# Kernel tuning notes

Measured on AMD Instinct MI355X. Metric: run time of the kernel, lower is better.

Reference implementation:

```python
import jax, jax.numpy as jnp
import numpy as np

N = 50000   # nodes
E = 800000  # edges (before self-loops)
IN = 128    # input feature dim
H = 4       # attention heads


def setup_inputs() -> dict:
    key = jax.random.key(0)
    ks = jax.random.split(key, 32)
    f = lambda k, s: (jax.random.normal(k, s, dtype=jnp.float32) * 0.1)
    inp = {
        "x": jax.random.normal(ks[0], (N, IN), dtype=jnp.float32),
        "edge_index": jax.random.randint(ks[1], (2, E), 0, N, dtype=jnp.int32),
        "edge_attr": jax.random.normal(ks[2], (E, 1), dtype=jnp.float32),
        # GATConv 1: 128 -> 8 per head, 4 heads (concat -> 32)
        "W1": f(ks[3], (IN, 32)), "as1": f(ks[4], (H, 8)), "ad1": f(ks[5], (H, 8)), "b1": jnp.zeros((32,), jnp.float32),
        # GATConv 2: 32 -> 16 per head (concat -> 64)
        "W2": f(ks[6], (32, 64)), "as2": f(ks[7], (H, 16)), "ad2": f(ks[8], (H, 16)), "b2": jnp.zeros((64,), jnp.float32),
        # GATConv 3: 64 -> 32 per head (concat -> 128)
        "W3": f(ks[9], (64, 128)), "as3": f(ks[10], (H, 32)), "ad3": f(ks[11], (H, 32)), "b3": jnp.zeros((128,), jnp.float32),
        # GATConv 4: 128 -> 64 per head (concat -> 256)
        "W4": f(ks[12], (128, 256)), "as4": f(ks[13], (H, 64)), "ad4": f(ks[14], (H, 64)), "b4": jnp.zeros((256,), jnp.float32),
        # MLP head
        "Wr": f(ks[15], (256, 32)), "br": jnp.zeros((32,), jnp.float32),
        "Wf1": f(ks[16], (32, 64)), "bf1": jnp.zeros((64,), jnp.float32),
        "Wf2": f(ks[17], (64, 1)), "bf2": jnp.zeros((1,), jnp.float32),
    }
    return inp


def _gat_layer(x, W, a_src, a_dst, bias, src, dst):
    """PyG GATConv (concat=True, negative_slope=0.2, self-loops appended upstream)."""
    heads, C = a_src.shape
    h = (x @ W).reshape(-1, heads, C)              # [N, H, C]
    alpha_s = jnp.sum(h * a_src[None], axis=-1)    # [N, H]
    alpha_d = jnp.sum(h * a_dst[None], axis=-1)    # [N, H]
    e = jax.nn.leaky_relu(alpha_s[src] + alpha_d[dst], 0.2)  # [E', H]
    # segment softmax over incoming edges of each destination node
    emax = jax.ops.segment_max(e, dst, num_segments=N)
    ee = jnp.exp(e - emax[dst])
    denom = jax.ops.segment_sum(ee, dst, num_segments=N)
    alpha = ee / denom[dst]                        # [E', H]
    msg = h[src] * alpha[:, :, None]               # [E', H, C]
    out = jax.ops.segment_sum(msg, dst, num_segments=N)  # [N, H, C]
    return out.reshape(-1, heads * C) + bias


def reference(x, edge_index, edge_attr,
              W1, as1, ad1, b1, W2, as2, ad2, b2,
              W3, as3, ad3, b3, W4, as4, ad4, b4,
              Wr, br, Wf1, bf1, Wf2, bf2):
    # edge_attr is accepted but unused, matching the original forward.
    loop = jnp.arange(N, dtype=edge_index.dtype)
    src = jnp.concatenate([edge_index[0], loop])   # add self-loops (PyG default)
    dst = jnp.concatenate([edge_index[1], loop])
    h = jax.nn.elu(_gat_layer(x, W1, as1, ad1, b1, src, dst))
    h = jax.nn.elu(_gat_layer(h, W2, as2, ad2, b2, src, dst))
    h = jax.nn.elu(_gat_layer(h, W3, as3, ad3, b3, src, dst))
    h = jax.nn.elu(_gat_layer(h, W4, as4, ad4, b4, src, dst))
    h = jax.nn.elu(h @ Wr + br)
    h = jax.nn.elu(h @ Wf1 + bf1)
    return h @ Wf2 + bf2                           # [N, 1]
```

## Files before the change

### kernel.cpp

```cpp
#include <hip/hip_runtime.h>
#include <hip/hip_fp16.h>
#include <math.h>

constexpr int NN = 50000;
constexpr int NE = 800000;
constexpr int NEP = NE + NN;
constexpr int CAP = 96;
constexpr int SCAT_B = (NEP + 255) / 256;
constexpr int PACK_B = 26;
constexpr int NT = (NN + 63) / 64;

typedef _Float16 half8_t __attribute__((ext_vector_type(8)));
typedef float    f32x4_t __attribute__((ext_vector_type(4)));

__device__ __forceinline__ float lrelu02(float x) { return x > 0.f ? x : 0.2f * x; }
__device__ __forceinline__ float eluf(float x)    { return x > 0.f ? x : (__expf(x) - 1.f); }
__device__ __forceinline__ float pick4(float4 q, int hd) {
  return (hd == 0) ? q.x : (hd == 1) ? q.y : (hd == 2) ? q.z : q.w;
}


__device__ __forceinline__ void pack_w_one(const float* __restrict__ W,
                                           __half* __restrict__ Wp,
                                           int M, int tid, int total) {
  if (tid >= total) return;
  int CT = M >> 4;
  int l = tid & 63;
  int c = (tid >> 6) % CT;
  int kc = (tid >> 6) / CT;
  int n = l & 15, q = l >> 4;
  __half* dst = Wp + (size_t)tid * 8;
  const float* src = W + (size_t)(kc * 32 + q * 8) * M + c * 16 + n;
  #pragma unroll
  for (int j = 0; j < 8; j++) dst[j] = __float2half_rn(src[j * M]);
}


template<int M, int C, int CT>
__device__ __forceinline__ void alpha_epilogue(const f32x4_t* acc,
    const float* __restrict__ a_src, const float* __restrict__ a_dst,
    int row_base, int m, float* __restrict__ as_out, float* __restrict__ ad_out) {
  float aS[CT], aD[CT];
  #pragma unroll
  for (int c = 0; c < CT; c++) { aS[c] = a_src[c * 16 + m]; aD[c] = a_dst[c * 16 + m]; }

  if constexpr (C == 8) {
    #pragma unroll
    for (int r = 0; r < 4; r++) {
      float p0 = acc[0][r] * aS[0], p1 = acc[1][r] * aS[1];
      float q0 = acc[0][r] * aD[0], q1 = acc[1][r] * aD[1];
      #pragma unroll
      for (int off = 1; off < 8; off <<= 1) {
        p0 += __shfl_xor(p0, off); p1 += __shfl_xor(p1, off);
        q0 += __shfl_xor(q0, off); q1 += __shfl_xor(q1, off);
      }
      int row = row_base + r;
      if ((m & 7) == 0 && row < NN) {
        int hb = m >> 3;
        as_out[row * 4 + hb]     = p0;
        as_out[row * 4 + 2 + hb] = p1;
        ad_out[row * 4 + hb]     = q0;
        ad_out[row * 4 + 2 + hb] = q1;
      }
    }
  } else {
    constexpr int FPH = C / 16;
    #pragma unroll
    for (int r = 0; r < 4; r++) {
      float bs[4] = {0.f, 0.f, 0.f, 0.f}, bd[4] = {0.f, 0.f, 0.f, 0.f};
      #pragma unroll
      for (int c = 0; c < CT; c++) {
        int hd = c / FPH;
        bs[hd] += acc[c][r] * aS[c];
        bd[hd] += acc[c][r] * aD[c];
      }
      #pragma unroll
      for (int off = 1; off < 16; off <<= 1)
        #pragma unroll
        for (int h = 0; h < 4; h++) {
          bs[h] += __shfl_xor(bs[h], off);
          bd[h] += __shfl_xor(bd[h], off);
        }
      int row = row_base + r;
      if (m < 4 && row < NN) {
        float vs = (m == 0) ? bs[0] : (m == 1) ? bs[1] : (m == 2) ? bs[2] : bs[3];
        float vd = (m == 0) ? bd[0] : (m == 1) ? bd[1] : (m == 2) ? bd[2] : bd[3];
        as_out[row * 4 + m] = vs;
        ad_out[row * 4 + m] = vd;
      }
    }
  }
}


__global__ __launch_bounds__(256) void front_kernel(
    const int* __restrict__ edge_src, const int* __restrict__ edge_dst,
    int* __restrict__ count, int* __restrict__ csr_src,
    const float* __restrict__ W1,
    const float* __restrict__ W2, __half* __restrict__ Wp2,
    const float* __restrict__ W3, __half* __restrict__ Wp3,
    const float* __restrict__ W4, __half* __restrict__ Wp4,
    const float* __restrict__ Wr, __half* __restrict__ Wrp,
    const float* __restrict__ Wf1, __half* __restrict__ Wf1p,
    const float* __restrict__ x, __half* __restrict__ Ch,
    const float* __restrict__ a_src, const float* __restrict__ a_dst,
    float* __restrict__ as_out, float* __restrict__ ad_out) {
  int b = blockIdx.x;
  if (b < SCAT_B) {
    int i = b * 256 + threadIdx.x;
    if (i < NEP) {
      int s, d;
      if (i < NE) { s = edge_src[i]; d = edge_dst[i]; } else { s = i - NE; d = s; }
      int pos = atomicAdd(&count[d], 1);
      if (pos < CAP) csr_src[d * CAP + pos] = s;
    }
    return;
  }
  if (b < SCAT_B + PACK_B) {
    int tid = (b - SCAT_B) * 256 + threadIdx.x;
    if (tid < 256)            pack_w_one(W2, Wp2, 64,  tid,        256);
    else if (tid < 1280)      pack_w_one(W3, Wp3, 128, tid - 256,  1024);
    else if (tid < 5376)      pack_w_one(W4, Wp4, 256, tid - 1280, 4096);
    else if (tid < 6400)      pack_w_one(Wr, Wrp, 32,  tid - 5376, 1024);
    else if (tid < 6656)      pack_w_one(Wf1, Wf1p, 64, tid - 6400, 256);
    return;
  }

  constexpr int M = 32, K = 128, CT = 2, KC = 4;
  __shared__ _Float16 Ah[64 * 40];
  __shared__ _Float16 Bs[KC * CT * 64 * 8];
  int t = threadIdx.x;
  int w = t >> 6, l = t & 63;
  int m = l & 15, q = l >> 4;
  int row0 = (b - SCAT_B - PACK_B) * 64;

  #pragma unroll
  for (int u0 = 0; u0 < 2; u0++) {
    int u = t + u0 * 256;
    int ul = u & 63;
    int uc = (u >> 6) & 1;
    int ukc = u >> 7;
    int un = ul & 15, uq = ul >> 4;
    const float* src = W1 + (size_t)(ukc * 32 + uq * 8) * M + uc * 16 + un;
    _Float16* dst = &Bs[u * 8];
    #pragma unroll
    for (int j = 0; j < 8; j++) dst[j] = (_Float16)src[j * M];
  }

  f32x4_t acc[CT];
  #pragma unroll
  for (int c = 0; c < CT; c++) acc[c] = (f32x4_t){0.f, 0.f, 0.f, 0.f};

  for (int kc = 0; kc < KC; kc++) {
    __syncthreads();
    #pragma unroll
    for (int i = 0; i < 2; i++) {
      int idx = t + 256 * i;
      int row = idx >> 3, c4 = idx & 7;
      int gr = row0 + row; if (gr >= NN) gr = NN - 1;
      float4 v = *(const float4*)(x + (size_t)gr * K + kc * 32 + c4 * 4);
      _Float16 h4[4] = {(_Float16)v.x, (_Float16)v.y, (_Float16)v.z, (_Float16)v.w};
      *(uint2*)(&Ah[row * 40 + c4 * 4]) = *(const uint2*)h4;
    }
    __syncthreads();
    half8_t a = *(const half8_t*)(&Ah[(w * 16 + m) * 40 + q * 8]);
    #pragma unroll
    for (int c = 0; c < CT; c++) {
      half8_t bf = *(const half8_t*)(&Bs[((kc * CT + c) * 64 + l) * 8]);
      acc[c] = __builtin_amdgcn_mfma_f32_16x16x32_f16(a, bf, acc[c], 0, 0, 0);
    }
  }

  #pragma unroll
  for (int r = 0; r < 4; r++) {
    int row = row0 + w * 16 + q * 4 + r;
    if (row < NN) {
      #pragma unroll
      for (int c = 0; c < CT; c++)
        Ch[(size_t)row * M + c * 16 + m] = __float2half_rn(acc[c][r]);
    }
  }
  alpha_epilogue<M, 8, CT>(acc, a_src, a_dst, row0 + w * 16 + q * 4, m, as_out, ad_out);
}


template<int M, int K, int C>
__global__ __launch_bounds__(256) void gemm_mfma_f16_kernel(const __half* __restrict__ A,
    const __half* __restrict__ Wp, __half* __restrict__ Ch,
    const float* __restrict__ a_src, const float* __restrict__ a_dst,
    float* __restrict__ as_out, float* __restrict__ ad_out) {
  constexpr int CT = M / 16;
  constexpr int KC = K / 32;
  __shared__ _Float16 Ah[64 * 40];
  int t = threadIdx.x;
  int w = t >> 6, l = t & 63;
  int m = l & 15, q = l >> 4;
  int row0 = blockIdx.x * 64;

  f32x4_t acc[CT];
  #pragma unroll
  for (int c = 0; c < CT; c++) acc[c] = (f32x4_t){0.f, 0.f, 0.f, 0.f};

  const half8_t* Bfrag = (const half8_t*)Wp;

  for (int kc = 0; kc < KC; kc++) {
    __syncthreads();
    {
      int row = t >> 2, c8 = t & 3;
      int gr = row0 + row; if (gr >= NN) gr = NN - 1;
      uint4 v = *(const uint4*)(A + (size_t)gr * K + kc * 32 + c8 * 8);
      *(uint4*)(&Ah[row * 40 + c8 * 8]) = v;
    }
    __syncthreads();
    half8_t a = *(const half8_t*)(&Ah[(w * 16 + m) * 40 + q * 8]);
    #pragma unroll
    for (int c = 0; c < CT; c++) {
      half8_t b = Bfrag[(kc * CT + c) * 64 + l];
      acc[c] = __builtin_amdgcn_mfma_f32_16x16x32_f16(a, b, acc[c], 0, 0, 0);
    }
  }

  #pragma unroll
  for (int r = 0; r < 4; r++) {
    int row = row0 + w * 16 + q * 4 + r;
    if (row < NN) {
      #pragma unroll
      for (int c = 0; c < CT; c++)
        Ch[(size_t)row * M + c * 16 + m] = __float2half_rn(acc[c][r]);
    }
  }
  alpha_epilogue<M, C, CT>(acc, a_src, a_dst, row0 + w * 16 + q * 4, m, as_out, ad_out);
}


template<int HC, int C>
__global__ __launch_bounds__(256) void agg_kernel(const __half* __restrict__ h,
    const float* __restrict__ as_v, const float* __restrict__ ad_v,
    const int* __restrict__ count, const int* __restrict__ csr_src,
    const float* __restrict__ bias, __half* __restrict__ out) {
  constexpr int V = HC / 8;
  constexpr int G = 64 / V;
  constexpr int P = 4;
  __shared__ float4 see4[4][CAP];
  __shared__ int    ssrc[4][CAP];
  int wid = threadIdx.x >> 6, lane = threadIdx.x & 63;
  int dst = blockIdx.x * 4 + wid;
  int base = dst * CAP;
  int deg = count[dst]; if (deg > CAP) deg = CAP;
  float4 ad = *(const float4*)(ad_v + dst * 4);

  float d0 = 0.f, d1 = 0.f, d2 = 0.f, d3 = 0.f;
  #pragma unroll
  for (int it = 0; it < 2; it++) {
    int j = lane + it * 64;
    if (j < deg) {
      int s = csr_src[base + j];
      float4 as = *(const float4*)(as_v + s * 4);
      float4 x = make_float4(__expf(lrelu02(as.x + ad.x)), __expf(lrelu02(as.y + ad.y)),
                             __expf(lrelu02(as.z + ad.z)), __expf(lrelu02(as.w + ad.w)));
      ssrc[wid][j] = s; see4[wid][j] = x;
      d0 += x.x; d1 += x.y; d2 += x.z; d3 += x.w;
    }
  }
  #pragma unroll
  for (int off = 32; off > 0; off >>= 1) {
    d0 += __shfl_xor(d0, off); d1 += __shfl_xor(d1, off);
    d2 += __shfl_xor(d2, off); d3 += __shfl_xor(d3, off);
  }
  float4 inv = make_float4(1.f / d0, 1.f / d1, 1.f / d2, 1.f / d3);

  int g = lane / V, v = lane % V;
  int hd = (v * 8) / C;
  float invh = pick4(inv, hd);
  int steps = (deg + G - 1) / G;
  const float4* hrows = (const float4*)h;

  float  px[P];
  float4 hv[P];
  #pragma unroll
  for (int k = 0; k < P; k++) {
    int jj = k * G + g;
    bool ok = jj < deg;
    int jc = ok ? jj : 0;
    int s = ssrc[wid][jc];
    float x = ((const float*)&see4[wid][jc])[hd];
    px[k] = ok ? x * invh : 0.f;
    hv[k] = hrows[(size_t)s * V + v];
  }

  float acc[8];
  #pragma unroll
  for (int i = 0; i < 8; i++) acc[i] = 0.f;
  int nB = (steps + P - 1) / P;
  for (int b = 1; b <= nB; b++) {
    #pragma unroll
    for (int k = 0; k < P; k++) {
      const __half2* hp = (const __half2*)&hv[k];
      float2 f0 = __half22float2(hp[0]);
      float2 f1 = __half22float2(hp[1]);
      float2 f2 = __half22float2(hp[2]);
      float2 f3 = __half22float2(hp[3]);
      float p = px[k];
      acc[0] += p * f0.x; acc[1] += p * f0.y;
      acc[2] += p * f1.x; acc[3] += p * f1.y;
      acc[4] += p * f2.x; acc[5] += p * f2.y;
      acc[6] += p * f3.x; acc[7] += p * f3.y;
      int jj = (b * P + k) * G + g;
      bool ok = jj < deg;
      int jc = ok ? jj : 0;
      int s = ssrc[wid][jc];
      float x = ((const float*)&see4[wid][jc])[hd];
      px[k] = ok ? x * invh : 0.f;
      hv[k] = hrows[(size_t)s * V + v];
    }
  }

  #pragma unroll
  for (int off = V; off < 64; off <<= 1)
    #pragma unroll
    for (int i = 0; i < 8; i++) acc[i] += __shfl_xor(acc[i], off);

  if (lane < V) {
    const float4* b4 = (const float4*)bias;
    float4 ba = b4[2 * v], bb = b4[2 * v + 1];
    _Float16 o[8];
    o[0] = (_Float16)eluf(acc[0] + ba.x); o[1] = (_Float16)eluf(acc[1] + ba.y);
    o[2] = (_Float16)eluf(acc[2] + ba.z); o[3] = (_Float16)eluf(acc[3] + ba.w);
    o[4] = (_Float16)eluf(acc[4] + bb.x); o[5] = (_Float16)eluf(acc[5] + bb.y);
    o[6] = (_Float16)eluf(acc[6] + bb.z); o[7] = (_Float16)eluf(acc[7] + bb.w);
    *(uint4*)(out + (size_t)dst * HC + v * 8) = *(const uint4*)o;
  }
}


__global__ __launch_bounds__(256) void mlp_mfma_kernel(const __half* __restrict__ h4,
    const __half* __restrict__ Wrp, const float* __restrict__ br,
    const __half* __restrict__ Wf1p, const float* __restrict__ bf1,
    const float* __restrict__ Wf2, const float* __restrict__ bf2,
    float* __restrict__ out) {
  __shared__ _Float16 rS[64 * 40];
  int t = threadIdx.x;
  int w = t >> 6, l = t & 63;
  int m = l & 15, q = l >> 4;
  int row0 = blockIdx.x * 64;
  const half8_t* Bwr  = (const half8_t*)Wrp;
  const half8_t* Bwf1 = (const half8_t*)Wf1p;

  int arow = row0 + w * 16 + m; if (arow >= NN) arow = NN - 1;
  const half8_t* Arow = (const half8_t*)(h4 + (size_t)arow * 256);
  half8_t afr[8];
  #pragma unroll
  for (int kc = 0; kc < 8; kc++) afr[kc] = Arow[kc * 4 + q];
  f32x4_t acc1[2];
  acc1[0] = (f32x4_t){0.f, 0.f, 0.f, 0.f};
  acc1[1] = (f32x4_t){0.f, 0.f, 0.f, 0.f};
  #pragma unroll
  for (int kc = 0; kc < 8; kc++) {
    acc1[0] = __builtin_amdgcn_mfma_f32_16x16x32_f16(afr[kc], Bwr[(kc * 2 + 0) * 64 + l], acc1[0], 0, 0, 0);
    acc1[1] = __builtin_amdgcn_mfma_f32_16x16x32_f16(afr[kc], Bwr[(kc * 2 + 1) * 64 + l], acc1[1], 0, 0, 0);
  }
  #pragma unroll
  for (int c = 0; c < 2; c++)
    #pragma unroll
    for (int r = 0; r < 4; r++) {
      float vv = eluf(acc1[c][r] + br[c * 16 + m]);
      rS[(w * 16 + q * 4 + r) * 40 + c * 16 + m] = (_Float16)vv;
    }
  __syncthreads();

  half8_t a2 = *(const half8_t*)(&rS[(w * 16 + m) * 40 + q * 8]);
  f32x4_t acc2[4];
  #pragma unroll
  for (int c = 0; c < 4; c++) acc2[c] = (f32x4_t){0.f, 0.f, 0.f, 0.f};
  #pragma unroll
  for (int c = 0; c < 4; c++)
    acc2[c] = __builtin_amdgcn_mfma_f32_16x16x32_f16(a2, Bwf1[c * 64 + l], acc2[c], 0, 0, 0);

  float wv[4] = {Wf2[m], Wf2[16 + m], Wf2[32 + m], Wf2[48 + m]};
  float rsum[4];
  #pragma unroll
  for (int r = 0; r < 4; r++) {
    float sr = 0.f;
    #pragma unroll
    for (int c = 0; c < 4; c++)
      sr += eluf(acc2[c][r] + bf1[c * 16 + m]) * wv[c];
    #pragma unroll
    for (int off = 1; off < 16; off <<= 1) sr += __shfl_xor(sr, off);
    rsum[r] = sr;
  }
  if (m == 0) {
    float b = bf2[0];
    #pragma unroll
    for (int r = 0; r < 4; r++) {
      int row = row0 + w * 16 + q * 4 + r;
      if (row < NN) out[row] = rsum[r] + b;
    }
  }
}


extern "C" void kernel_launch(void* const* d_in, const int* in_sizes, int n_in,
                              void* d_out, int out_size, void* d_ws, size_t ws_size,
                              hipStream_t stream) {
  const float* x   = (const float*)d_in[0];
  const int*   ei  = (const int*)d_in[1];
  const float* W1  = (const float*)d_in[3];
  const float* as1 = (const float*)d_in[4];
  const float* ad1 = (const float*)d_in[5];
  const float* b1  = (const float*)d_in[6];
  const float* W2  = (const float*)d_in[7];
  const float* as2 = (const float*)d_in[8];
  const float* ad2 = (const float*)d_in[9];
  const float* b2  = (const float*)d_in[10];
  const float* W3  = (const float*)d_in[11];
  const float* as3 = (const float*)d_in[12];
  const float* ad3 = (const float*)d_in[13];
  const float* b3  = (const float*)d_in[14];
  const float* W4  = (const float*)d_in[15];
  const float* as4 = (const float*)d_in[16];
  const float* ad4 = (const float*)d_in[17];
  const float* b4  = (const float*)d_in[18];
  const float* Wr  = (const float*)d_in[19];
  const float* br  = (const float*)d_in[20];
  const float* Wf1 = (const float*)d_in[21];
  const float* bf1 = (const float*)d_in[22];
  const float* Wf2 = (const float*)d_in[23];
  const float* bf2 = (const float*)d_in[24];
  float* out = (float*)d_out;

  char* p = (char*)d_ws;
  auto alloc = [&](size_t bytes) {
    char* q = p;
    p += (bytes + 255) & ~(size_t)255;
    return q;
  };
  int* count   = (int*)alloc((size_t)NN * 4);
  int* csr_src = (int*)alloc((size_t)NN * CAP * 4);
  __half* Hh = (__half*)alloc((size_t)NN * 256 * 2);
  __half* B2 = (__half*)alloc((size_t)NN * 128 * 2);
  __half* B3 = (__half*)alloc((size_t)NN * 256 * 2);
  float* as_buf = (float*)alloc((size_t)NN * 4 * 4);
  float* ad_buf = (float*)alloc((size_t)NN * 4 * 4);
  __half* Wp2 = (__half*)alloc((size_t)32 * 64 * 2);
  __half* Wp3 = (__half*)alloc((size_t)64 * 128 * 2);
  __half* Wp4 = (__half*)alloc((size_t)128 * 256 * 2);
  __half* Wrp = (__half*)alloc((size_t)256 * 32 * 2);
  __half* Wf1p = (__half*)alloc((size_t)32 * 64 * 2);

  const int* edge_src = ei;
  const int* edge_dst = ei + NE;

  hipMemsetAsync(count, 0, (size_t)NN * 4, stream);
  front_kernel<<<SCAT_B + PACK_B + NT, 256, 0, stream>>>(
      edge_src, edge_dst, count, csr_src,
      W1, W2, Wp2, W3, Wp3, W4, Wp4, Wr, Wrp, Wf1, Wf1p,
      x, Hh, as1, ad1, as_buf, ad_buf);

  int gb  = NT;
  int ggb = NN / 4;

  agg_kernel<32, 8><<<ggb, 256, 0, stream>>>(Hh, as_buf, ad_buf, count, csr_src, b1, B2);

  gemm_mfma_f16_kernel<64, 32, 16><<<gb, 256, 0, stream>>>(B2, Wp2, Hh, as2, ad2, as_buf, ad_buf);
  agg_kernel<64, 16><<<ggb, 256, 0, stream>>>(Hh, as_buf, ad_buf, count, csr_src, b2, B3);

  gemm_mfma_f16_kernel<128, 64, 32><<<gb, 256, 0, stream>>>(B3, Wp3, Hh, as3, ad3, as_buf, ad_buf);
  agg_kernel<128, 32><<<ggb, 256, 0, stream>>>(Hh, as_buf, ad_buf, count, csr_src, b3, B2);

  gemm_mfma_f16_kernel<256, 128, 64><<<gb, 256, 0, stream>>>(B2, Wp4, Hh, as4, ad4, as_buf, ad_buf);
  agg_kernel<256, 64><<<ggb, 256, 0, stream>>>(Hh, as_buf, ad_buf, count, csr_src, b4, B3);

  mlp_mfma_kernel<<<gb, 256, 0, stream>>>(B3, Wrp, br, Wf1p, bf1, Wf2, bf2, out);
}
```

Measured before the change: 403.4 us.

## Fuse each aggregation with the following layer GEMM and the MLP head

Each aggregation kernel is merged with the next layer's MFMA GEMM (and the last one with the MLP head). Each block of 64 rows aggregates 16 destinations per wave, writes the results to a staging buffer, syncs, then runs the GEMM on those rows. This removes four kernel launches and the inter-kernel gaps. Ping-pong buffers keep a fused kernel from overwriting its own inputs. The cost is much lower parallelism in the gather phase: each wave now processes 16 nodes one after another instead of one node per wave across many blocks. The prefetch depth also rises from 4 to 8, which may raise register pressure.

```diff
diff --git a/kernel.cpp b/kernel.cpp
--- a/kernel.cpp
+++ b/kernel.cpp
@@ -184,128 +184,51 @@
 }
 
 
-template<int M, int K, int C>
-__global__ __launch_bounds__(256) void gemm_mfma_f16_kernel(const __half* __restrict__ A,
-    const __half* __restrict__ Wp, __half* __restrict__ Ch,
-    const float* __restrict__ a_src, const float* __restrict__ a_dst,
-    float* __restrict__ as_out, float* __restrict__ ad_out) {
-  constexpr int CT = M / 16;
-  constexpr int KC = K / 32;
-  __shared__ _Float16 Ah[64 * 40];
-  int t = threadIdx.x;
-  int w = t >> 6, l = t & 63;
-  int m = l & 15, q = l >> 4;
-  int row0 = blockIdx.x * 64;
-
-  f32x4_t acc[CT];
-  #pragma unroll
-  for (int c = 0; c < CT; c++) acc[c] = (f32x4_t){0.f, 0.f, 0.f, 0.f};
-
-  const half8_t* Bfrag = (const half8_t*)Wp;
-
-  for (int kc = 0; kc < KC; kc++) {
-    __syncthreads();
-    {
-      int row = t >> 2, c8 = t & 3;
-      int gr = row0 + row; if (gr >= NN) gr = NN - 1;
-      uint4 v = *(const uint4*)(A + (size_t)gr * K + kc * 32 + c8 * 8);
-      *(uint4*)(&Ah[row * 40 + c8 * 8]) = v;
-    }
-    __syncthreads();
-    half8_t a = *(const half8_t*)(&Ah[(w * 16 + m) * 40 + q * 8]);
-    #pragma unroll
-    for (int c = 0; c < CT; c++) {
-      half8_t b = Bfrag[(kc * CT + c) * 64 + l];
-      acc[c] = __builtin_amdgcn_mfma_f32_16x16x32_f16(a, b, acc[c], 0, 0, 0);
-    }
-  }
-
-  #pragma unroll
-  for (int r = 0; r < 4; r++) {
-    int row = row0 + w * 16 + q * 4 + r;
-    if (row < NN) {
-      #pragma unroll
-      for (int c = 0; c < CT; c++)
-        Ch[(size_t)row * M + c * 16 + m] = __float2half_rn(acc[c][r]);
-    }
-  }
-  alpha_epilogue<M, C, CT>(acc, a_src, a_dst, row0 + w * 16 + q * 4, m, as_out, ad_out);
-}
-
-
 template<int HC, int C>
-__global__ __launch_bounds__(256) void agg_kernel(const __half* __restrict__ h,
+__device__ __forceinline__ void agg16_phase(const __half* __restrict__ h,
     const float* __restrict__ as_v, const float* __restrict__ ad_v,
     const int* __restrict__ count, const int* __restrict__ csr_src,
-    const float* __restrict__ bias, __half* __restrict__ out) {
+    const float* __restrict__ bias, __half* __restrict__ S,
+    float4 (*see4)[CAP], int (*ssrc)[CAP], int row0, int wid, int lane) {
   constexpr int V = HC / 8;
   constexpr int G = 64 / V;
-  constexpr int P = 4;
-  __shared__ float4 see4[4][CAP];
-  __shared__ int    ssrc[4][CAP];
-  int wid = threadIdx.x >> 6, lane = threadIdx.x & 63;
-  int dst = blockIdx.x * 4 + wid;
-  int base = dst * CAP;
-  int deg = count[dst]; if (deg > CAP) deg = CAP;
-  float4 ad = *(const float4*)(ad_v + dst * 4);
-
-  float d0 = 0.f, d1 = 0.f, d2 = 0.f, d3 = 0.f;
-  #pragma unroll
-  for (int it = 0; it < 2; it++) {
-    int j = lane + it * 64;
-    if (j < deg) {
-      int s = csr_src[base + j];
-      float4 as = *(const float4*)(as_v + s * 4);
-      float4 x = make_float4(__expf(lrelu02(as.x + ad.x)), __expf(lrelu02(as.y + ad.y)),
-                             __expf(lrelu02(as.z + ad.z)), __expf(lrelu02(as.w + ad.w)));
-      ssrc[wid][j] = s; see4[wid][j] = x;
-      d0 += x.x; d1 += x.y; d2 += x.z; d3 += x.w;
-    }
-  }
-  #pragma unroll
-  for (int off = 32; off > 0; off >>= 1) {
-    d0 += __shfl_xor(d0, off); d1 += __shfl_xor(d1, off);
-    d2 += __shfl_xor(d2, off); d3 += __shfl_xor(d3, off);
-  }
-  float4 inv = make_float4(1.f / d0, 1.f / d1, 1.f / d2, 1.f / d3);
-
+  constexpr int P = 8;
   int g = lane / V, v = lane % V;
   int hd = (v * 8) / C;
-  float invh = pick4(inv, hd);
-  int steps = (deg + G - 1) / G;
   const float4* hrows = (const float4*)h;
 
-  float  px[P];
-  float4 hv[P];
-  #pragma unroll
-  for (int k = 0; k < P; k++) {
-    int jj = k * G + g;
-    bool ok = jj < deg;
-    int jc = ok ? jj : 0;
-    int s = ssrc[wid][jc];
-    float x = ((const float*)&see4[wid][jc])[hd];
-    px[k] = ok ? x * invh : 0.f;
-    hv[k] = hrows[(size_t)s * V + v];
-  }
-
-  float acc[8];
-  #pragma unroll
-  for (int i = 0; i < 8; i++) acc[i] = 0.f;
-  int nB = (steps + P - 1) / P;
-  for (int b = 1; b <= nB; b++) {
+  for (int n = 0; n < 16; n++) {
+    int dst = row0 + wid * 16 + n; if (dst >= NN) dst = NN - 1;
+    int base = dst * CAP;
+    int deg = count[dst]; if (deg > CAP) deg = CAP;
+    float4 ad = *(const float4*)(ad_v + dst * 4);
+
+    float d0 = 0.f, d1 = 0.f, d2 = 0.f, d3 = 0.f;
+    #pragma unroll
+    for (int it = 0; it < 2; it++) {
+      int j = lane + it * 64;
+      if (j < deg) {
+        int s = csr_src[base + j];
+        float4 as = *(const float4*)(as_v + s * 4);
+        float4 x = make_float4(__expf(lrelu02(as.x + ad.x)), __expf(lrelu02(as.y + ad.y)),
+                               __expf(lrelu02(as.z + ad.z)), __expf(lrelu02(as.w + ad.w)));
+        ssrc[wid][j] = s; see4[wid][j] = x;
+        d0 += x.x; d1 += x.y; d2 += x.z; d3 += x.w;
+      }
+    }
+    #pragma unroll
+    for (int off = 32; off > 0; off >>= 1) {
+      d0 += __shfl_xor(d0, off); d1 += __shfl_xor(d1, off);
+      d2 += __shfl_xor(d2, off); d3 += __shfl_xor(d3, off);
+    }
+    float4 inv4 = make_float4(1.f / d0, 1.f / d1, 1.f / d2, 1.f / d3);
+    float invh = pick4(inv4, hd);
+
+    float  px[P];
+    float4 hv[P];
     #pragma unroll
     for (int k = 0; k < P; k++) {
-      const __half2* hp = (const __half2*)&hv[k];
-      float2 f0 = __half22float2(hp[0]);
-      float2 f1 = __half22float2(hp[1]);
-      float2 f2 = __half22float2(hp[2]);
-      float2 f3 = __half22float2(hp[3]);
-      float p = px[k];
-      acc[0] += p * f0.x; acc[1] += p * f0.y;
-      acc[2] += p * f1.x; acc[3] += p * f1.y;
-      acc[4] += p * f2.x; acc[5] += p * f2.y;
-      acc[6] += p * f3.x; acc[7] += p * f3.y;
-      int jj = (b * P + k) * G + g;
+      int jj = k * G + g;
       bool ok = jj < deg;
       int jc = ok ? jj : 0;
       int s = ssrc[wid][jc];
@@ -313,41 +236,132 @@
       px[k] = ok ? x * invh : 0.f;
       hv[k] = hrows[(size_t)s * V + v];
     }
-  }
-
-  #pragma unroll
-  for (int off = V; off < 64; off <<= 1)
-    #pragma unroll
-    for (int i = 0; i < 8; i++) acc[i] += __shfl_xor(acc[i], off);
-
-  if (lane < V) {
-    const float4* b4 = (const float4*)bias;
-    float4 ba = b4[2 * v], bb = b4[2 * v + 1];
-    _Float16 o[8];
-    o[0] = (_Float16)eluf(acc[0] + ba.x); o[1] = (_Float16)eluf(acc[1] + ba.y);
-    o[2] = (_Float16)eluf(acc[2] + ba.z); o[3] = (_Float16)eluf(acc[3] + ba.w);
-    o[4] = (_Float16)eluf(acc[4] + bb.x); o[5] = (_Float16)eluf(acc[5] + bb.y);
-    o[6] = (_Float16)eluf(acc[6] + bb.z); o[7] = (_Float16)eluf(acc[7] + bb.w);
-    *(uint4*)(out + (size_t)dst * HC + v * 8) = *(const uint4*)o;
-  }
-}
-
-
-__global__ __launch_bounds__(256) void mlp_mfma_kernel(const __half* __restrict__ h4,
+    float acc[8];
+    #pragma unroll
+    for (int i = 0; i < 8; i++) acc[i] = 0.f;
+    int steps = (deg + G - 1) / G;
+    int nB = (steps + P - 1) / P;
+    for (int b = 1; b <= nB; b++) {
+      #pragma unroll
+      for (int k = 0; k < P; k++) {
+        const __half2* hp = (const __half2*)&hv[k];
+        float2 f0 = __half22float2(hp[0]);
+        float2 f1 = __half22float2(hp[1]);
+        float2 f2 = __half22float2(hp[2]);
+        float2 f3 = __half22float2(hp[3]);
+        float p = px[k];
+        acc[0] += p * f0.x; acc[1] += p * f0.y;
+        acc[2] += p * f1.x; acc[3] += p * f1.y;
+        acc[4] += p * f2.x; acc[5] += p * f2.y;
+        acc[6] += p * f3.x; acc[7] += p * f3.y;
+        int jj = (b * P + k) * G + g;
+        bool ok = jj < deg;
+        int jc = ok ? jj : 0;
+        int s = ssrc[wid][jc];
+        float x = ((const float*)&see4[wid][jc])[hd];
+        px[k] = ok ? x * invh : 0.f;
+        hv[k] = hrows[(size_t)s * V + v];
+      }
+    }
+    #pragma unroll
+    for (int off = V; off < 64; off <<= 1)
+      #pragma unroll
+      for (int i = 0; i < 8; i++) acc[i] += __shfl_xor(acc[i], off);
+
+    if (lane < V) {
+      const float4* b4p = (const float4*)bias;
+      float4 ba = b4p[2 * v], bb = b4p[2 * v + 1];
+      _Float16 o[8];
+      o[0] = (_Float16)eluf(acc[0] + ba.x); o[1] = (_Float16)eluf(acc[1] + ba.y);
+      o[2] = (_Float16)eluf(acc[2] + ba.z); o[3] = (_Float16)eluf(acc[3] + ba.w);
+      o[4] = (_Float16)eluf(acc[4] + bb.x); o[5] = (_Float16)eluf(acc[5] + bb.y);
+      o[6] = (_Float16)eluf(acc[6] + bb.z); o[7] = (_Float16)eluf(acc[7] + bb.w);
+      *(uint4*)(S + (size_t)dst * HC + v * 8) = *(const uint4*)o;
+    }
+  }
+}
+
+
+template<int HC, int C, int M>
+__global__ __launch_bounds__(256) void agg_gemm_kernel(const __half* __restrict__ h,
+    const float* __restrict__ as_v, const float* __restrict__ ad_v,
+    const int* __restrict__ count, const int* __restrict__ csr_src,
+    const float* __restrict__ bias, __half* __restrict__ S,
+    const __half* __restrict__ Wp, __half* __restrict__ Ch,
+    const float* __restrict__ a_src, const float* __restrict__ a_dst,
+    float* __restrict__ as_out, float* __restrict__ ad_out) {
+  constexpr int CT = M / 16;
+  constexpr int KC = HC / 32;
+  __shared__ __align__(16) char smem[7680];
+  float4 (*see4)[CAP] = (float4 (*)[CAP])smem;
+  int    (*ssrc)[CAP] = (int (*)[CAP])(smem + 6144);
+  _Float16* Ah = (_Float16*)smem;
+  int t = threadIdx.x, wid = t >> 6, lane = t & 63;
+  int row0 = blockIdx.x * 64;
+
+  agg16_phase<HC, C>(h, as_v, ad_v, count, csr_src, bias, S, see4, ssrc, row0, wid, lane);
+  __syncthreads();
+
+  int m = lane & 15, q = lane >> 4;
+  f32x4_t acc[CT];
+  #pragma unroll
+  for (int c = 0; c < CT; c++) acc[c] = (f32x4_t){0.f, 0.f, 0.f, 0.f};
+  const half8_t* Bfrag = (const half8_t*)Wp;
+
+  for (int kc = 0; kc < KC; kc++) {
+    __syncthreads();
+    {
+      int row = t >> 2, c8 = t & 3;
+      int gr = row0 + row; if (gr >= NN) gr = NN - 1;
+      uint4 v = *(const uint4*)(S + (size_t)gr * HC + kc * 32 + c8 * 8);
+      *(uint4*)(&Ah[row * 40 + c8 * 8]) = v;
+    }
+    __syncthreads();
+    half8_t a = *(const half8_t*)(&Ah[(wid * 16 + m) * 40 + q * 8]);
+    #pragma unroll
+    for (int c = 0; c < CT; c++) {
+      half8_t b = Bfrag[(kc * CT + c) * 64 + lane];
+      acc[c] = __builtin_amdgcn_mfma_f32_16x16x32_f16(a, b, acc[c], 0, 0, 0);
+    }
+  }
+
+  #pragma unroll
+  for (int r = 0; r < 4; r++) {
+    int row = row0 + wid * 16 + q * 4 + r;
+    if (row < NN) {
+      #pragma unroll
+      for (int c = 0; c < CT; c++)
+        Ch[(size_t)row * M + c * 16 + m] = __float2half_rn(acc[c][r]);
+    }
+  }
+  alpha_epilogue<M, M / 4, CT>(acc, a_src, a_dst, row0 + wid * 16 + q * 4, m, as_out, ad_out);
+}
+
+
+__global__ __launch_bounds__(256) void agg_mlp_kernel(const __half* __restrict__ h,
+    const float* __restrict__ as_v, const float* __restrict__ ad_v,
+    const int* __restrict__ count, const int* __restrict__ csr_src,
+    const float* __restrict__ bias, __half* __restrict__ S,
     const __half* __restrict__ Wrp, const float* __restrict__ br,
     const __half* __restrict__ Wf1p, const float* __restrict__ bf1,
     const float* __restrict__ Wf2, const float* __restrict__ bf2,
     float* __restrict__ out) {
-  __shared__ _Float16 rS[64 * 40];
-  int t = threadIdx.x;
-  int w = t >> 6, l = t & 63;
-  int m = l & 15, q = l >> 4;
+  __shared__ __align__(16) char smem[7680];
+  float4 (*see4)[CAP] = (float4 (*)[CAP])smem;
+  int    (*ssrc)[CAP] = (int (*)[CAP])(smem + 6144);
+  _Float16* rS = (_Float16*)smem;
+  int t = threadIdx.x, wid = t >> 6, lane = t & 63;
   int row0 = blockIdx.x * 64;
+
+  agg16_phase<256, 64>(h, as_v, ad_v, count, csr_src, bias, S, see4, ssrc, row0, wid, lane);
+  __syncthreads();
+
+  int m = lane & 15, q = lane >> 4;
   const half8_t* Bwr  = (const half8_t*)Wrp;
   const half8_t* Bwf1 = (const half8_t*)Wf1p;
 
-  int arow = row0 + w * 16 + m; if (arow >= NN) arow = NN - 1;
-  const half8_t* Arow = (const half8_t*)(h4 + (size_t)arow * 256);
+  int arow = row0 + wid * 16 + m; if (arow >= NN) arow = NN - 1;
+  const half8_t* Arow = (const half8_t*)(S + (size_t)arow * 256);
   half8_t afr[8];
   #pragma unroll
   for (int kc = 0; kc < 8; kc++) afr[kc] = Arow[kc * 4 + q];
@@ -356,25 +370,25 @@
   acc1[1] = (f32x4_t){0.f, 0.f, 0.f, 0.f};
   #pragma unroll
   for (int kc = 0; kc < 8; kc++) {
-    acc1[0] = __builtin_amdgcn_mfma_f32_16x16x32_f16(afr[kc], Bwr[(kc * 2 + 0) * 64 + l], acc1[0], 0, 0, 0);
-    acc1[1] = __builtin_amdgcn_mfma_f32_16x16x32_f16(afr[kc], Bwr[(kc * 2 + 1) * 64 + l], acc1[1], 0, 0, 0);
+    acc1[0] = __builtin_amdgcn_mfma_f32_16x16x32_f16(afr[kc], Bwr[(kc * 2 + 0) * 64 + lane], acc1[0], 0, 0, 0);
+    acc1[1] = __builtin_amdgcn_mfma_f32_16x16x32_f16(afr[kc], Bwr[(kc * 2 + 1) * 64 + lane], acc1[1], 0, 0, 0);
   }
   #pragma unroll
   for (int c = 0; c < 2; c++)
     #pragma unroll
     for (int r = 0; r < 4; r++) {
       float vv = eluf(acc1[c][r] + br[c * 16 + m]);
-      rS[(w * 16 + q * 4 + r) * 40 + c * 16 + m] = (_Float16)vv;
+      rS[(wid * 16 + q * 4 + r) * 40 + c * 16 + m] = (_Float16)vv;
     }
   __syncthreads();
 
-  half8_t a2 = *(const half8_t*)(&rS[(w * 16 + m) * 40 + q * 8]);
+  half8_t a2 = *(const half8_t*)(&rS[(wid * 16 + m) * 40 + q * 8]);
   f32x4_t acc2[4];
   #pragma unroll
   for (int c = 0; c < 4; c++) acc2[c] = (f32x4_t){0.f, 0.f, 0.f, 0.f};
   #pragma unroll
   for (int c = 0; c < 4; c++)
-    acc2[c] = __builtin_amdgcn_mfma_f32_16x16x32_f16(a2, Bwf1[c * 64 + l], acc2[c], 0, 0, 0);
+    acc2[c] = __builtin_amdgcn_mfma_f32_16x16x32_f16(a2, Bwf1[c * 64 + lane], acc2[c], 0, 0, 0);
 
   float wv[4] = {Wf2[m], Wf2[16 + m], Wf2[32 + m], Wf2[48 + m]};
   float rsum[4];
@@ -392,7 +406,7 @@
     float b = bf2[0];
     #pragma unroll
     for (int r = 0; r < 4; r++) {
-      int row = row0 + w * 16 + q * 4 + r;
+      int row = row0 + wid * 16 + q * 4 + r;
       if (row < NN) out[row] = rsum[r] + b;
     }
   }
@@ -436,11 +450,13 @@
   };
   int* count   = (int*)alloc((size_t)NN * 4);
   int* csr_src = (int*)alloc((size_t)NN * CAP * 4);
-  __half* Hh = (__half*)alloc((size_t)NN * 256 * 2);
-  __half* B2 = (__half*)alloc((size_t)NN * 128 * 2);
-  __half* B3 = (__half*)alloc((size_t)NN * 256 * 2);
-  float* as_buf = (float*)alloc((size_t)NN * 4 * 4);
-  float* ad_buf = (float*)alloc((size_t)NN * 4 * 4);
+  __half* bufA = (__half*)alloc((size_t)NN * 256 * 2);
+  __half* bufB = (__half*)alloc((size_t)NN * 256 * 2);
+  __half* Sbuf = (__half*)alloc((size_t)NN * 256 * 2);
+  float* as_a = (float*)alloc((size_t)NN * 4 * 4);
+  float* ad_a = (float*)alloc((size_t)NN * 4 * 4);
+  float* as_b = (float*)alloc((size_t)NN * 4 * 4);
+  float* ad_b = (float*)alloc((size_t)NN * 4 * 4);
   __half* Wp2 = (__half*)alloc((size_t)32 * 64 * 2);
   __half* Wp3 = (__half*)alloc((size_t)64 * 128 * 2);
   __half* Wp4 = (__half*)alloc((size_t)128 * 256 * 2);
@@ -454,21 +470,14 @@
   front_kernel<<<SCAT_B + PACK_B + NT, 256, 0, stream>>>(
       edge_src, edge_dst, count, csr_src,
       W1, W2, Wp2, W3, Wp3, W4, Wp4, Wr, Wrp, Wf1, Wf1p,
-      x, Hh, as1, ad1, as_buf, ad_buf);
-
-  int gb  = NT;
-  int ggb = NN / 4;
-
-  agg_kernel<32, 8><<<ggb, 256, 0, stream>>>(Hh, as_buf, ad_buf, count, csr_src, b1, B2);
-
-  gemm_mfma_f16_kernel<64, 32, 16><<<gb, 256, 0, stream>>>(B2, Wp2, Hh, as2, ad2, as_buf, ad_buf);
-  agg_kernel<64, 16><<<ggb, 256, 0, stream>>>(Hh, as_buf, ad_buf, count, csr_src, b2, B3);
-
-  gemm_mfma_f16_kernel<128, 64, 32><<<gb, 256, 0, stream>>>(B3, Wp3, Hh, as3, ad3, as_buf, ad_buf);
-  agg_kernel<128, 32><<<ggb, 256, 0, stream>>>(Hh, as_buf, ad_buf, count, csr_src, b3, B2);
-
-  gemm_mfma_f16_kernel<256, 128, 64><<<gb, 256, 0, stream>>>(B2, Wp4, Hh, as4, ad4, as_buf, ad_buf);
-  agg_kernel<256, 64><<<ggb, 256, 0, stream>>>(Hh, as_buf, ad_buf, count, csr_src, b4, B3);
-
-  mlp_mfma_kernel<<<gb, 256, 0, stream>>>(B3, Wrp, br, Wf1p, bf1, Wf2, bf2, out);
-}
+      x, bufA, as1, ad1, as_a, ad_a);
+
+  agg_gemm_kernel<32, 8, 64><<<NT, 256, 0, stream>>>(
+      bufA, as_a, ad_a, count, csr_src, b1, Sbuf, Wp2, bufB, as2, ad2, as_b, ad_b);
+  agg_gemm_kernel<64, 16, 128><<<NT, 256, 0, stream>>>(
+      bufB, as_b, ad_b, count, csr_src, b2, Sbuf, Wp3, bufA, as3, ad3, as_a, ad_a);
+  agg_gemm_kernel<128, 32, 256><<<NT, 256, 0, stream>>>(
+      bufA, as_a, ad_a, count, csr_src, b3, Sbuf, Wp4, bufB, as4, ad4, as_b, ad_b);
+  agg_mlp_kernel<<<NT, 256, 0, stream>>>(
+      bufB, as_b, ad_b, count, csr_src, b4, Sbuf, Wrp, br, Wf1p, bf1, Wf2, bf2, out);
+}
```

Measured after the change: 561.9 us. 39.3% more time.
